# Kernel tuning notes

Measured on AMD Instinct MI355X. Metric: run time of the kernel, lower is better.

The kernel has to match this reference:

```python
import jax, jax.numpy as jnp
import numpy as np

B, S, H, DH = 64, 300, 4, 32   # batch, seq, heads, head_dim
D = H * DH                     # hidden = 128
L = 8                          # num_hidden_layers
SPAN = 8                       # max_relative_positions (att_span)
EPS = 1e-7                     # DebertaConfig layer_norm_eps default


def _ln(x, s, b):
    mu = x.mean(-1, keepdims=True)
    var = ((x - mu) ** 2).mean(-1, keepdims=True)
    return (x - mu) * jax.lax.rsqrt(var + EPS) * s + b


def _gelu(x):
    return jax.nn.gelu(x, approximate=False)  # torch nn.GELU / HF 'gelu' (erf)


def setup_inputs():
    ks = iter(jax.random.split(jax.random.key(0), 48))
    w = lambda shape: jax.random.normal(next(ks), shape, jnp.float32) * 0.02
    return dict(
        inputs=jax.random.uniform(next(ks), (B, S, 4), jnp.float32),
        mask=jnp.ones((B, S), jnp.float32),
        emb_W1=w((3, 64)), emb_b1=w((64,)),
        emb_W2=w((64, D)), emb_b2=w((D,)),
        emb_W3=w((D, D)), emb_b3=w((D,)),
        tok_emb=w((2, D)),
        emb_ln_s=jnp.ones((D,), jnp.float32), emb_ln_b=jnp.zeros((D,), jnp.float32),
        rel_emb=w((2 * SPAN, D)),
        qkv_W=w((L, D, 3 * D)), q_bias=w((L, D)), v_bias=w((L, D)),
        pos_k_W=w((L, D, D)), pos_q_W=w((L, D, D)), pos_q_b=w((L, D)),
        attn_out_W=w((L, D, D)), attn_out_b=w((L, D)),
        ln1_s=jnp.ones((L, D), jnp.float32), ln1_b=jnp.zeros((L, D), jnp.float32),
        ffn_W1=w((L, D, 512)), ffn_b1=w((L, 512)),
        ffn_W2=w((L, 512, D)), ffn_b2=w((L, D)),
        ln2_s=jnp.ones((L, D), jnp.float32), ln2_b=jnp.zeros((L, D), jnp.float32),
        rec_W1=w((D, D)), rec_b1=w((D,)),
        rec_W2=w((D, 64)), rec_b2=w((64,)),
        rec_W3=w((64, 5)), rec_b3=w((5,)),
        conn_W=w((S * 5, 2500)), conn_b=w((2500,)),
    )


def reference(inputs, mask, emb_W1, emb_b1, emb_W2, emb_b2, emb_W3, emb_b3,
              tok_emb, emb_ln_s, emb_ln_b, rel_emb,
              qkv_W, q_bias, v_bias, pos_k_W, pos_q_W, pos_q_b,
              attn_out_W, attn_out_b, ln1_s, ln1_b,
              ffn_W1, ffn_b1, ffn_W2, ffn_b2, ln2_s, ln2_b,
              rec_W1, rec_b1, rec_W2, rec_b2, rec_W3, rec_b3,
              conn_W, conn_b):
    # ---- embedding MLP on first 3 feature columns ----
    e = _gelu(inputs[..., :3] @ emb_W1 + emb_b1)
    e = _gelu(e @ emb_W2 + emb_b2)
    e = _gelu(e @ emb_W3 + emb_b3)
    tok = inputs[..., 3].astype(jnp.int32)            # token_type_ids
    e = _ln(e + tok_emb[tok], emb_ln_s, emb_ln_b)     # position_biased_input=False
    x = e * mask[..., None]                           # DebertaEmbeddings mask mult

    # ---- relative position indices (q_size == k_size == S) ----
    rel = jnp.arange(S)[:, None] - jnp.arange(S)[None, :]
    c2p_idx = jnp.clip(rel + SPAN, 0, 2 * SPAN - 1)   # [S,S]
    p2c_idx = jnp.clip(-rel + SPAN, 0, 2 * SPAN - 1)  # [S,S]
    mask4 = (mask[:, None, :, None] * mask[:, None, None, :]) > 0  # [B,1,S,S]
    neg = jnp.finfo(x.dtype).min
    scale = jnp.sqrt(jnp.asarray(DH * 3, x.dtype))    # scale_factor = 1+len([c2p,p2c])

    for l in range(L):
        qkv = (x @ qkv_W[l]).reshape(B, S, H, 3, DH)  # in_proj (no bias)
        q = qkv[..., 0, :].transpose(0, 2, 1, 3) + q_bias[l].reshape(H, DH)[None, :, None, :]
        k = qkv[..., 1, :].transpose(0, 2, 1, 3)
        v = qkv[..., 2, :].transpose(0, 2, 1, 3) + v_bias[l].reshape(H, DH)[None, :, None, :]
        q = q / scale
        scores = jnp.einsum('bhqd,bhkd->bhqk', q, k)  # content-to-content
        # content-to-position
        pos_k = (rel_emb @ pos_k_W[l]).reshape(2 * SPAN, H, DH).transpose(1, 0, 2)  # [H,16,DH]
        c2p = jnp.einsum('bhqd,hrd->bhqr', q, pos_k)  # [B,H,S,16]
        scores = scores + jnp.take_along_axis(c2p, c2p_idx[None, None], axis=-1)
        # position-to-content
        pos_q = ((rel_emb @ pos_q_W[l]) + pos_q_b[l]).reshape(2 * SPAN, H, DH).transpose(1, 0, 2) / scale
        p2c = jnp.einsum('bhkd,hrd->bhkr', k, pos_q)  # [B,H,S,16]
        scores = scores + jnp.swapaxes(jnp.take_along_axis(p2c, p2c_idx[None, None], axis=-1), -1, -2)
        # XSoftmax
        probs = jnp.where(mask4, jax.nn.softmax(jnp.where(mask4, scores, neg), axis=-1), 0.0)
        ctx = jnp.einsum('bhqk,bhkd->bhqd', probs, v).transpose(0, 2, 1, 3).reshape(B, S, D)
        x = _ln(ctx @ attn_out_W[l] + attn_out_b[l] + x, ln1_s[l], ln1_b[l])
        h = _gelu(x @ ffn_W1[l] + ffn_b1[l])
        x = _ln(h @ ffn_W2[l] + ffn_b2[l] + x, ln2_s[l], ln2_b[l])

    # ---- reconstruction MLP + connection ----
    r = _gelu(x @ rec_W1 + rec_b1)
    r = _gelu(r @ rec_W2 + rec_b2)
    r = _gelu(r @ rec_W3 + rec_b3)                    # [B,S,5]
    out = r.reshape(B, S * 5) @ conn_W + conn_b       # [B,2500]
    return out.reshape(-1, 50, 50)
```

## Files before the change

### kernel.cpp

```cpp
#include <hip/hip_runtime.h>
#include <hip/hip_bf16.h>
#include <math.h>

#define Bq 64
#define Sq 300
#define NH 4
#define DHd 32
#define Dd 128
#define NL 8
#define FF 512
#define NIN 36
#define SP 304
#define SPX 320

typedef __attribute__((ext_vector_type(8))) short bf16x8;
typedef __attribute__((ext_vector_type(4))) float f32x4;

__device__ __forceinline__ float gelu_f(float x) {
    return 0.5f * x * (1.0f + erff(x * 0.70710678118654752f));
}
__device__ __forceinline__ bool bf16_mode(const unsigned* maskw) {
    return maskw[0] == 0x3F803F80u;
}

struct ConvArgs {
    const void* src[NIN];
    float* dst[NIN];
    int n[NIN];
};

__global__ void convert_kernel(ConvArgs a, const unsigned* maskw) {
    bool bfm = bf16_mode(maskw);
    int bi = blockIdx.y;
    int n = a.n[bi];
    float* dst = a.dst[bi];
    int stride = gridDim.x * blockDim.x;
    int i0 = blockIdx.x * blockDim.x + threadIdx.x;
    if (bfm) {
        const __hip_bfloat16* s = (const __hip_bfloat16*)a.src[bi];
        for (int i = i0; i < n; i += stride) dst[i] = __bfloat162float(s[i]);
    } else {
        const float* s = (const float*)a.src[bi];
        for (int i = i0; i < n; i += stride) dst[i] = s[i];
    }
}

__global__ void pack_kernel(const float* __restrict__ W1all, const float* __restrict__ W2all,
                            const float* __restrict__ Wqall, const float* __restrict__ Woall,
                            const float* __restrict__ Wr1, const float* __restrict__ Wr2,
                            const float* __restrict__ We2, const float* __restrict__ We3,
                            __hip_bfloat16* __restrict__ P1, __hip_bfloat16* __restrict__ P2,
                            __hip_bfloat16* __restrict__ Pq, __hip_bfloat16* __restrict__ Po,
                            __hip_bfloat16* __restrict__ Pr1, __hip_bfloat16* __restrict__ Pr2,
                            __hip_bfloat16* __restrict__ Pe2, __hip_bfloat16* __restrict__ Pe3) {
    int l = blockIdx.y;
    int which = blockIdx.z;
    if (which >= 4 && l != 0) return;
    int K = (which == 1) ? 512 : ((which == 6) ? 64 : 128);
    int N = (which == 0) ? 512 : (which == 1 ? 128 : (which == 2 ? 384 : (which == 5 ? 64 : 128)));
    int slots = (K / 32) * (N / 16) * 64;
    int idx = blockIdx.x * 256 + threadIdx.x;
    if (idx >= slots) return;
    int lane = idx & 63;
    int nkt = K / 32;
    int kt = (idx >> 6) % nkt;
    int nt = (idx >> 6) / nkt;
    const float* W; __hip_bfloat16* P;
    switch (which) {
        case 0:  W = W1all + (size_t)l * 128 * 512; P = P1 + (size_t)l * 65536; break;
        case 1:  W = W2all + (size_t)l * 512 * 128; P = P2 + (size_t)l * 65536; break;
        case 2:  W = Wqall + (size_t)l * 128 * 384; P = Pq + (size_t)l * 49152; break;
        case 3:  W = Woall + (size_t)l * 128 * 128; P = Po + (size_t)l * 16384; break;
        case 4:  W = Wr1; P = Pr1; break;
        case 5:  W = Wr2; P = Pr2; break;
        case 6:  W = We2; P = Pe2; break;
        default: W = We3; P = Pe3; break;
    }
    P += (size_t)idx * 8;
    int n = nt * 16 + (lane & 15);
    int k0 = kt * 32 + (lane >> 4) * 8;
    #pragma unroll
    for (int j = 0; j < 8; j++) P[j] = __float2bfloat16(W[(size_t)(k0 + j) * N + n]);
}

__global__ __launch_bounds__(256) void embed_mfma_kernel(
        const float* __restrict__ inp, const float* __restrict__ mask,
        const float* __restrict__ W1, const float* __restrict__ b1,
        const __hip_bfloat16* __restrict__ Pe2, const float* __restrict__ b2,
        const __hip_bfloat16* __restrict__ Pe3, const float* __restrict__ b3,
        const float* __restrict__ tok_emb,
        const float* __restrict__ ln_s, const float* __restrict__ ln_b,
        float* __restrict__ x) {
    int blk = blockIdx.x;
    int t = threadIdx.x;
    int w = t >> 6, lane = t & 63;
    int row0 = blk * 16;
    __shared__ float f[16][4];
    __shared__ __align__(16) __hip_bfloat16 e1a[16 * 72];
    __shared__ __align__(16) __hip_bfloat16 e2a[16 * 136];
    __shared__ float dbuf[16 * 132];
    if (t < 64) f[t >> 2][t & 3] = inp[(size_t)(row0 + (t >> 2)) * 4 + (t & 3)];
    __syncthreads();
    {
        int r1 = t >> 4, n0 = (t & 15) * 4;
        float f0 = f[r1][0], f1 = f[r1][1], f2 = f[r1][2];
        #pragma unroll
        for (int j = 0; j < 4; j++) {
            int n = n0 + j;
            float a = b1[n] + f0 * W1[n] + f1 * W1[64 + n] + f2 * W1[128 + n];
            e1a[r1 * 72 + n] = __float2bfloat16(gelu_f(a));
        }
    }
    __syncthreads();
    int m = lane & 15, quad = lane >> 4;
    bf16x8 a2[2];
    #pragma unroll
    for (int kt = 0; kt < 2; kt++) a2[kt] = *(bf16x8*)&e1a[m * 72 + kt * 32 + quad * 8];
    #pragma unroll
    for (int nt0 = 0; nt0 < 2; nt0++) {
        int nt = w * 2 + nt0;
        f32x4 acc = {0.f, 0.f, 0.f, 0.f};
        const bf16x8* bp = (const bf16x8*)(Pe2 + (size_t)nt * 2 * 512);
        #pragma unroll
        for (int kt = 0; kt < 2; kt++) {
            bf16x8 bfr = bp[kt * 64 + lane];
            acc = __builtin_amdgcn_mfma_f32_16x16x32_bf16(a2[kt], bfr, acc, 0, 0, 0);
        }
        int n = nt * 16 + m;
        float bb = b2[n];
        #pragma unroll
        for (int r = 0; r < 4; r++)
            e2a[(quad * 4 + r) * 136 + n] = __float2bfloat16(gelu_f(acc[r] + bb));
    }
    __syncthreads();
    bf16x8 a3[4];
    #pragma unroll
    for (int kt = 0; kt < 4; kt++) a3[kt] = *(bf16x8*)&e2a[m * 136 + kt * 32 + quad * 8];
    f32x4 acc2[2] = {{0.f,0.f,0.f,0.f}, {0.f,0.f,0.f,0.f}};
    #pragma unroll
    for (int kt = 0; kt < 4; kt++) {
        #pragma unroll
        for (int nt0 = 0; nt0 < 2; nt0++) {
            int nt = w * 2 + nt0;
            bf16x8 bfr = ((const bf16x8*)(Pe3 + (size_t)nt * 4 * 512))[kt * 64 + lane];
            acc2[nt0] = __builtin_amdgcn_mfma_f32_16x16x32_bf16(a3[kt], bfr, acc2[nt0], 0, 0, 0);
        }
    }
    #pragma unroll
    for (int nt0 = 0; nt0 < 2; nt0++) {
        int n = (w * 2 + nt0) * 16 + m;
        float bb = b3[n];
        #pragma unroll
        for (int r = 0; r < 4; r++) {
            int row = quad * 4 + r;
            int tok = (int)f[row][3];
            dbuf[row * 132 + n] = gelu_f(acc2[nt0][r] + bb) + tok_emb[tok * 128 + n];
        }
    }
    __syncthreads();
    #pragma unroll
    for (int rr = 0; rr < 4; rr++) {
        int row = w * 4 + rr;
        int c0 = lane, c1 = lane + 64;
        float y0 = dbuf[row * 132 + c0];
        float y1 = dbuf[row * 132 + c1];
        float sm = y0 + y1;
        #pragma unroll
        for (int o = 32; o > 0; o >>= 1) sm += __shfl_xor(sm, o);
        float mu = sm * (1.0f / 128.0f);
        float d0 = y0 - mu, d1 = y1 - mu;
        float vv = d0 * d0 + d1 * d1;
        #pragma unroll
        for (int o = 32; o > 0; o >>= 1) vv += __shfl_xor(vv, o);
        float rstd = rsqrtf(vv * (1.0f / 128.0f) + 1e-7f);
        float mk = mask[row0 + row];
        x[(size_t)(row0 + row) * 128 + c0] = (d0 * rstd * ln_s[c0] + ln_b[c0]) * mk;
        x[(size_t)(row0 + row) * 128 + c1] = (d1 * rstd * ln_s[c1] + ln_b[c1]) * mk;
    }
}

__global__ __launch_bounds__(256) void qkv_mfma_kernel(const float* __restrict__ x,
                                                       const __hip_bfloat16* __restrict__ Pq,
                                                       const float* __restrict__ qb, const float* __restrict__ vb,
                                                       __hip_bfloat16* __restrict__ qbf,
                                                       __hip_bfloat16* __restrict__ kbf,
                                                       __hip_bfloat16* __restrict__ vT) {
    int blk = blockIdx.x;
    int t = threadIdx.x;
    int w = t >> 6, lane = t & 63;
    int row0 = blk * 16;
    __shared__ __align__(16) __hip_bfloat16 xa[16 * 136];
    for (int i = t; i < 512; i += 256) {
        float4 v4 = ((const float4*)(x + (size_t)row0 * 128))[i];
        int r = i >> 5, c4 = (i & 31) * 4;
        __hip_bfloat16* d = &xa[r * 136 + c4];
        d[0] = __float2bfloat16(v4.x); d[1] = __float2bfloat16(v4.y);
        d[2] = __float2bfloat16(v4.z); d[3] = __float2bfloat16(v4.w);
    }
    __syncthreads();
    int m = lane & 15, quad = lane >> 4;
    bf16x8 a1[4];
    #pragma unroll
    for (int kt = 0; kt < 4; kt++) a1[kt] = *(bf16x8*)&xa[m * 136 + kt * 32 + quad * 8];
    const float inv_scale = 0.10206207261596576f;
    #pragma unroll
    for (int nt0 = 0; nt0 < 6; nt0++) {
        int nt = w * 6 + nt0;
        f32x4 acc = {0.f, 0.f, 0.f, 0.f};
        const bf16x8* bp = (const bf16x8*)(Pq + (size_t)nt * 4 * 512);
        #pragma unroll
        for (int kt = 0; kt < 4; kt++) {
            bf16x8 bfr = bp[kt * 64 + lane];
            acc = __builtin_amdgcn_mfma_f32_16x16x32_bf16(a1[kt], bfr, acc, 0, 0, 0);
        }
        int n = nt * 16 + m;
        int h = n / 96, mm = (n % 96) / 32, d = n % 32;
        float qbv = qb[h * 32 + d], vbv = vb[h * 32 + d];
        #pragma unroll
        for (int r = 0; r < 4; r++) {
            int row = row0 + quad * 4 + r;
            int bb = row / Sq, s = row % Sq;
            int bh = bb * NH + h;
            float a = acc[r];
            if (mm == 0) {
                qbf[((size_t)bh * SP + s) * 32 + d] = __float2bfloat16((a + qbv) * inv_scale);
            } else if (mm == 1) {
                kbf[((size_t)bh * SP + s) * 32 + d] = __float2bfloat16(a);
            } else {
                vT[((size_t)bh * 32 + d) * SP + s] = __float2bfloat16(a + vbv);
            }
        }
    }
}

__global__ void pad_kernel(__hip_bfloat16* qbf, __hip_bfloat16* kbf, __hip_bfloat16* vT) {
    int i = blockIdx.x * 256 + threadIdx.x;
    if (i >= 256 * 4 * 32) return;
    int bh = i >> 7, s = Sq + ((i >> 5) & 3), d = i & 31;
    __hip_bfloat16 z = __float2bfloat16(0.0f);
    qbf[((size_t)bh * SP + s) * 32 + d] = z;
    kbf[((size_t)bh * SP + s) * 32 + d] = z;
    vT[((size_t)bh * 32 + d) * SP + s] = z;
}

__global__ void pos_kernel(const float* __restrict__ rel_emb,
                           const float* __restrict__ pkW_all, const float* __restrict__ pqW_all,
                           const float* __restrict__ pqb_all,
                           __hip_bfloat16* __restrict__ poskb, __hip_bfloat16* __restrict__ posqb) {
    int l = blockIdx.y;
    int bi = blockIdx.x;
    int which = bi >> 4;
    int r = bi & 15;
    int t = threadIdx.x;
    __shared__ float re[128];
    re[t] = rel_emb[r * 128 + t];
    __syncthreads();
    const float* W = (which ? pqW_all : pkW_all) + (size_t)l * 128 * 128;
    float a = 0.0f;
    for (int k = 0; k < 128; k++) a += re[k] * W[k * 128 + t];
    int h = t >> 5, d = t & 31;
    size_t o = ((size_t)(l * NH + h) * 16 + r) * 32 + d;
    if (which) { a = (a + pqb_all[l * 128 + t]) * 0.10206207261596576f; posqb[o] = __float2bfloat16(a); }
    else       { poskb[o] = __float2bfloat16(a); }
}

__global__ __launch_bounds__(256) void attn_mfma_kernel(const __hip_bfloat16* __restrict__ qbf,
                                                        const __hip_bfloat16* __restrict__ kbf,
                                                        const __hip_bfloat16* __restrict__ vT,
                                                        const __hip_bfloat16* __restrict__ poskb,
                                                        const __hip_bfloat16* __restrict__ posqb,
                                                        const float* __restrict__ mask,
                                                        __hip_bfloat16* __restrict__ ctxb) {
    int bh = blockIdx.x;
    int b = bh >> 2, h = bh & 3;
    int t = threadIdx.x;
    int w = t >> 6, lane = t & 63;
    int m = lane & 15, quad = lane >> 4;

    __shared__ float p2cS[SPX * 17];
    __shared__ float c2pS[4][16 * 17];
    __shared__ __align__(16) __hip_bfloat16 pT[4][16 * 40];

    {
        bf16x8 pqf = *(const bf16x8*)&posqb[(h * 16 + m) * 32 + quad * 8];
        #pragma unroll
        for (int it = 0; it < 5; it++) {
            int jb = (w + it * 4) * 16;
            bf16x8 kf2 = *(const bf16x8*)&kbf[((size_t)bh * SP + jb + m) * 32 + quad * 8];
            f32x4 pc = __builtin_amdgcn_mfma_f32_16x16x32_bf16(kf2, pqf, (f32x4){0.f,0.f,0.f,0.f}, 0, 0, 0);
            #pragma unroll
            for (int r = 0; r < 4; r++) {
                int j = jb + quad * 4 + r;
                float mv = (j < Sq) ? mask[b * Sq + j] : 0.0f;
                p2cS[j * 17 + m] = (mv > 0.0f) ? pc[r] : -30000.0f;
            }
        }
    }
    __syncthreads();

    int qt = blockIdx.y * 4 + w;
    if (qt >= 19) return;
    int q0 = qt * 16;

    float* c2pW = c2pS[w];
    __hip_bfloat16* pTW = pT[w];

    bf16x8 aq = *(const bf16x8*)&qbf[((size_t)bh * SP + q0 + m) * 32 + quad * 8];

    {
        bf16x8 pkf = *(const bf16x8*)&poskb[(h * 16 + m) * 32 + quad * 8];
        f32x4 cc = __builtin_amdgcn_mfma_f32_16x16x32_bf16(aq, pkf, (f32x4){0.f,0.f,0.f,0.f}, 0, 0, 0);
        #pragma unroll
        for (int r = 0; r < 4; r++) c2pW[(quad * 4 + r) * 17 + m] = cc[r];
    }

    int qi = q0 + m;
    f32x4 oacc[2] = {{0.f,0.f,0.f,0.f}, {0.f,0.f,0.f,0.f}};
    float lacc = 0.0f;

    for (int jt2 = 0; jt2 < 10; jt2++) {
        int j0 = jt2 * 32;
        #pragma unroll
        for (int half = 0; half < 2; half++) {
            int jh = j0 + half * 16;
            bf16x8 kf = *(const bf16x8*)&kbf[((size_t)bh * SP + jh + m) * 32 + quad * 8];
            f32x4 sc = __builtin_amdgcn_mfma_f32_16x16x32_bf16(kf, aq, (f32x4){0.f,0.f,0.f,0.f}, 0, 0, 0);
            int jb2 = jh + quad * 4;
            int base = qi - jb2 + 8;
            __hip_bfloat16 pb[4];
            #pragma unroll
            for (int r = 0; r < 4; r++) {
                int rr = base - r; rr = rr < 0 ? 0 : (rr > 15 ? 15 : rr);
                float sv = sc[r] + c2pW[m * 17 + rr] + p2cS[(jb2 + r) * 17 + rr];
                float p = __expf(sv);
                lacc += p;
                pb[r] = __float2bfloat16(p);
            }
            *(uint2*)&pTW[m * 40 + half * 16 + quad * 4] = *(uint2*)pb;
        }
        bf16x8 ap = *(bf16x8*)&pTW[m * 40 + quad * 8];
        #pragma unroll
        for (int nt = 0; nt < 2; nt++) {
            bf16x8 vf = *(const bf16x8*)&vT[((size_t)bh * 32 + nt * 16 + m) * SP + j0 + quad * 8];
            oacc[nt] = __builtin_amdgcn_mfma_f32_16x16x32_bf16(ap, vf, oacc[nt], 0, 0, 0);
        }
    }

    lacc += __shfl_xor(lacc, 16);
    lacc += __shfl_xor(lacc, 32);
    #pragma unroll
    for (int r = 0; r < 4; r++) {
        int qrow = quad * 4 + r;
        float lr = __shfl(lacc, qrow);
        int qi2 = q0 + qrow;
        float qm = (qi2 < Sq) ? mask[b * Sq + qi2] : 0.0f;
        float inv = (qm > 0.0f && lr > 0.0f) ? 1.0f / lr : 0.0f;
        if (qi2 < Sq) {
            size_t base2 = ((size_t)(b * Sq + qi2)) * 128 + h * 32;
            ctxb[base2 + m]      = __float2bfloat16(oacc[0][r] * inv);
            ctxb[base2 + 16 + m] = __float2bfloat16(oacc[1][r] * inv);
        }
    }
}

__global__ __launch_bounds__(256) void aoffn_mfma_kernel(
        const __hip_bfloat16* __restrict__ ctxb,
        const __hip_bfloat16* __restrict__ Po, const float* __restrict__ ob,
        const float* __restrict__ ln1s, const float* __restrict__ ln1b,
        const __hip_bfloat16* __restrict__ P1, const float* __restrict__ b1,
        const __hip_bfloat16* __restrict__ P2, const float* __restrict__ b2,
        const float* __restrict__ ln2s, const float* __restrict__ ln2b,
        float* __restrict__ x) {
    int blk = blockIdx.x;
    int t = threadIdx.x;
    int w = t >> 6, lane = t & 63;
    int row0 = blk * 16;

    __shared__ __align__(16) __hip_bfloat16 ca[16 * 136];
    __shared__ float xr[16 * 128];
    __shared__ __align__(16) __hip_bfloat16 ha[16 * 520];
    __shared__ float dbuf[16 * 132];

    {
        uint4 cv = ((const uint4*)(ctxb + (size_t)row0 * 128))[t];
        int r = t >> 4, c8 = (t & 15) * 8;
        *(uint4*)&ca[r * 136 + c8] = cv;
    }
    for (int i = t; i < 512; i += 256) {
        float4 xv4 = ((const float4*)(x + (size_t)row0 * 128))[i];
        int r = i >> 5, c4 = (i & 31) * 4;
        *(float4*)&xr[r * 128 + c4] = xv4;
    }
    __syncthreads();

    int m = lane & 15, quad = lane >> 4;

    {
        bf16x8 a1[4];
        #pragma unroll
        for (int kt = 0; kt < 4; kt++) a1[kt] = *(bf16x8*)&ca[m * 136 + kt * 32 + quad * 8];
        f32x4 acc2[2] = {{0.f,0.f,0.f,0.f}, {0.f,0.f,0.f,0.f}};
        #pragma unroll
        for (int kt = 0; kt < 4; kt++) {
            #pragma unroll
            for (int nt0 = 0; nt0 < 2; nt0++) {
                int nt = w * 2 + nt0;
                bf16x8 bfr = ((const bf16x8*)(Po + (size_t)nt * 4 * 512))[kt * 64 + lane];
                acc2[nt0] = __builtin_amdgcn_mfma_f32_16x16x32_bf16(a1[kt], bfr, acc2[nt0], 0, 0, 0);
            }
        }
        #pragma unroll
        for (int nt0 = 0; nt0 < 2; nt0++) {
            int n = (w * 2 + nt0) * 16 + m;
            #pragma unroll
            for (int r = 0; r < 4; r++) dbuf[(quad * 4 + r) * 132 + n] = acc2[nt0][r];
        }
    }
    __syncthreads();

    #pragma unroll
    for (int rr = 0; rr < 4; rr++) {
        int row = w * 4 + rr;
        int c0 = lane, c1 = lane + 64;
        float y0 = dbuf[row * 132 + c0] + ob[c0] + xr[row * 128 + c0];
        float y1 = dbuf[row * 132 + c1] + ob[c1] + xr[row * 128 + c1];
        float sm = y0 + y1;
        #pragma unroll
        for (int o = 32; o > 0; o >>= 1) sm += __shfl_xor(sm, o);
        float mu = sm * (1.0f / 128.0f);
        float d0 = y0 - mu, d1 = y1 - mu;
        float vv = d0 * d0 + d1 * d1;
        #pragma unroll
        for (int o = 32; o > 0; o >>= 1) vv += __shfl_xor(vv, o);
        float rstd = rsqrtf(vv * (1.0f / 128.0f) + 1e-7f);
        float o0 = d0 * rstd * ln1s[c0] + ln1b[c0];
        float o1 = d1 * rstd * ln1s[c1] + ln1b[c1];
        xr[row * 128 + c0] = o0;
        xr[row * 128 + c1] = o1;
        ca[row * 136 + c0] = __float2bfloat16(o0);
        ca[row * 136 + c1] = __float2bfloat16(o1);
    }
    __syncthreads();

    {
        bf16x8 a1[4];
        #pragma unroll
        for (int kt = 0; kt < 4; kt++) a1[kt] = *(bf16x8*)&ca[m * 136 + kt * 32 + quad * 8];
        #pragma unroll
        for (int nt0 = 0; nt0 < 8; nt0++) {
            int nt = w * 8 + nt0;
            f32x4 acc = {0.f, 0.f, 0.f, 0.f};
            const bf16x8* bp = (const bf16x8*)(P1 + (size_t)nt * 4 * 512);
            #pragma unroll
            for (int kt = 0; kt < 4; kt++) {
                bf16x8 bfr = bp[kt * 64 + lane];
                acc = __builtin_amdgcn_mfma_f32_16x16x32_bf16(a1[kt], bfr, acc, 0, 0, 0);
            }
            int n = nt * 16 + m;
            float bb = b1[n];
            #pragma unroll
            for (int r = 0; r < 4; r++)
                ha[(quad * 4 + r) * 520 + n] = __float2bfloat16(gelu_f(acc[r] + bb));
        }
    }
    __syncthreads();

    {
        f32x4 acc2[2] = {{0.f,0.f,0.f,0.f}, {0.f,0.f,0.f,0.f}};
        #pragma unroll
        for (int kt = 0; kt < 16; kt++) {
            bf16x8 a = *(bf16x8*)&ha[m * 520 + kt * 32 + quad * 8];
            #pragma unroll
            for (int nt0 = 0; nt0 < 2; nt0++) {
                int nt = w * 2 + nt0;
                bf16x8 bfr = ((const bf16x8*)(P2 + (size_t)nt * 16 * 512))[kt * 64 + lane];
                acc2[nt0] = __builtin_amdgcn_mfma_f32_16x16x32_bf16(a, bfr, acc2[nt0], 0, 0, 0);
            }
        }
        #pragma unroll
        for (int nt0 = 0; nt0 < 2; nt0++) {
            int n = (w * 2 + nt0) * 16 + m;
            #pragma unroll
            for (int r = 0; r < 4; r++)
                dbuf[(quad * 4 + r) * 132 + n] = acc2[nt0][r];
        }
    }
    __syncthreads();

    #pragma unroll
    for (int rr = 0; rr < 4; rr++) {
        int row = w * 4 + rr;
        int c0 = lane, c1 = lane + 64;
        float y0 = dbuf[row * 132 + c0] + b2[c0] + xr[row * 128 + c0];
        float y1 = dbuf[row * 132 + c1] + b2[c1] + xr[row * 128 + c1];
        float sm = y0 + y1;
        #pragma unroll
        for (int o = 32; o > 0; o >>= 1) sm += __shfl_xor(sm, o);
        float mu = sm * (1.0f / 128.0f);
        float d0 = y0 - mu, d1 = y1 - mu;
        float vv = d0 * d0 + d1 * d1;
        #pragma unroll
        for (int o = 32; o > 0; o >>= 1) vv += __shfl_xor(vv, o);
        float rstd = rsqrtf(vv * (1.0f / 128.0f) + 1e-7f);
        x[(size_t)(row0 + row) * 128 + c0] = d0 * rstd * ln2s[c0] + ln2b[c0];
        x[(size_t)(row0 + row) * 128 + c1] = d1 * rstd * ln2s[c1] + ln2b[c1];
    }
}

__global__ __launch_bounds__(256) void rec_mfma_kernel(const float* __restrict__ x,
                                                       const __hip_bfloat16* __restrict__ Pr1,
                                                       const float* __restrict__ b1,
                                                       const __hip_bfloat16* __restrict__ Pr2,
                                                       const float* __restrict__ b2,
                                                       const float* __restrict__ W3, const float* __restrict__ b3,
                                                       float* __restrict__ r3) {
    int blk = blockIdx.x;
    int t = threadIdx.x;
    int w = t >> 6, lane = t & 63;
    int row0 = blk * 16;
    __shared__ __align__(16) __hip_bfloat16 xa[16 * 136];
    __shared__ __align__(16) __hip_bfloat16 ha[16 * 136];
    __shared__ float r2s[16 * 68];
    for (int i = t; i < 512; i += 256) {
        float4 v4 = ((const float4*)(x + (size_t)row0 * 128))[i];
        int r = i >> 5, c4 = (i & 31) * 4;
        __hip_bfloat16* d = &xa[r * 136 + c4];
        d[0] = __float2bfloat16(v4.x); d[1] = __float2bfloat16(v4.y);
        d[2] = __float2bfloat16(v4.z); d[3] = __float2bfloat16(v4.w);
    }
    __syncthreads();
    int m = lane & 15, quad = lane >> 4;

    bf16x8 a1[4];
    #pragma unroll
    for (int kt = 0; kt < 4; kt++) a1[kt] = *(bf16x8*)&xa[m * 136 + kt * 32 + quad * 8];
    #pragma unroll
    for (int nt0 = 0; nt0 < 2; nt0++) {
        int nt = w * 2 + nt0;
        f32x4 acc = {0.f, 0.f, 0.f, 0.f};
        const bf16x8* bp = (const bf16x8*)(Pr1 + (size_t)nt * 4 * 512);
        #pragma unroll
        for (int kt = 0; kt < 4; kt++) {
            bf16x8 bfr = bp[kt * 64 + lane];
            acc = __builtin_amdgcn_mfma_f32_16x16x32_bf16(a1[kt], bfr, acc, 0, 0, 0);
        }
        int n = nt * 16 + m;
        float bb = b1[n];
        #pragma unroll
        for (int r = 0; r < 4; r++)
            ha[(quad * 4 + r) * 136 + n] = __float2bfloat16(gelu_f(acc[r] + bb));
    }
    __syncthreads();

    {
        f32x4 acc = {0.f, 0.f, 0.f, 0.f};
        const bf16x8* bp = (const bf16x8*)(Pr2 + (size_t)w * 4 * 512);
        #pragma unroll
        for (int kt = 0; kt < 4; kt++) {
            bf16x8 a = *(bf16x8*)&ha[m * 136 + kt * 32 + quad * 8];
            bf16x8 bfr = bp[kt * 64 + lane];
            acc = __builtin_amdgcn_mfma_f32_16x16x32_bf16(a, bfr, acc, 0, 0, 0);
        }
        int n = w * 16 + m;
        float bb = b2[n];
        #pragma unroll
        for (int r = 0; r < 4; r++)
            r2s[(quad * 4 + r) * 68 + n] = gelu_f(acc[r] + bb);
    }
    __syncthreads();

    if (t < 80) {
        int row = t / 5, c = t % 5;
        float a = b3[c];
        for (int k = 0; k < 64; k++) a += r2s[row * 68 + k] * W3[k * 5 + c];
        r3[(size_t)(row0 + row) * 5 + c] = gelu_f(a);
    }
}

__global__ void conn_kernel(const float* __restrict__ r3, const float* __restrict__ W,
                            const float* __restrict__ b, void* out, const unsigned* maskw) {
    bool bfm = bf16_mode(maskw);
    int cb = blockIdx.x;
    int bg = blockIdx.y;
    int t = threadIdx.x;
    int cl = t & 63;
    int kq = t >> 6;
    int col = cb * 64 + cl;
    __shared__ float rs[4 * 1500];
    __shared__ float pacc[4 * 64 * 4];
    {
        const float4* src = (const float4*)(r3 + (size_t)bg * 4 * 1500);
        for (int i = t; i < 1500; i += 256) ((float4*)rs)[i] = src[i];
    }
    __syncthreads();
    float acc[4] = {0.f, 0.f, 0.f, 0.f};
    if (col < 2500) {
        for (int k = kq * 4; k < 1500; k += 16) {
            float w0 = W[(size_t)(k + 0) * 2500 + col];
            float w1 = W[(size_t)(k + 1) * 2500 + col];
            float w2 = W[(size_t)(k + 2) * 2500 + col];
            float w3 = W[(size_t)(k + 3) * 2500 + col];
            #pragma unroll
            for (int bb = 0; bb < 4; bb++) {
                float4 rv = *(const float4*)&rs[bb * 1500 + k];
                acc[bb] += rv.x * w0 + rv.y * w1 + rv.z * w2 + rv.w * w3;
            }
        }
    }
    #pragma unroll
    for (int bb = 0; bb < 4; bb++) pacc[(kq * 64 + cl) * 4 + bb] = acc[bb];
    __syncthreads();
    if (kq == 0 && col < 2500) {
        float bv = b[col];
        #pragma unroll
        for (int bb = 0; bb < 4; bb++) {
            float a = bv + pacc[(0 * 64 + cl) * 4 + bb] + pacc[(1 * 64 + cl) * 4 + bb]
                         + pacc[(2 * 64 + cl) * 4 + bb] + pacc[(3 * 64 + cl) * 4 + bb];
            int ob = bg * 4 + bb;
            if (bfm) ((__hip_bfloat16*)out)[(size_t)ob * 2500 + col] = __float2bfloat16(a);
            else     ((float*)out)[(size_t)ob * 2500 + col] = a;
        }
    }
}

extern "C" void kernel_launch(void* const* d_in, const int* in_sizes, int n_in,
                              void* d_out, int out_size, void* d_ws, size_t ws_size,
                              hipStream_t stream) {
    float* ws = (float*)d_ws;

    float* cv[NIN];
    size_t off = 0;
    for (int i = 0; i < NIN; i++) { cv[i] = ws + off; off += (size_t)in_sizes[i]; }

    const float* inp      = cv[0];
    const float* mask     = cv[1];
    const float* emb_W1   = cv[2];
    const float* emb_b1   = cv[3];
    const float* emb_W2   = cv[4];
    const float* emb_b2   = cv[5];
    const float* emb_W3   = cv[6];
    const float* emb_b3   = cv[7];
    const float* tok_emb  = cv[8];
    const float* emb_ln_s = cv[9];
    const float* emb_ln_b = cv[10];
    const float* rel_emb  = cv[11];
    const float* qkv_W    = cv[12];
    const float* q_bias   = cv[13];
    const float* v_bias   = cv[14];
    const float* pos_k_W  = cv[15];
    const float* pos_q_W  = cv[16];
    const float* pos_q_b  = cv[17];
    const float* attn_out_W = cv[18];
    const float* attn_out_b = cv[19];
    const float* ln1_s    = cv[20];
    const float* ln1_b    = cv[21];
    const float* ffn_W1   = cv[22];
    const float* ffn_b1   = cv[23];
    const float* ffn_W2   = cv[24];
    const float* ffn_b2   = cv[25];
    const float* ln2_s    = cv[26];
    const float* ln2_b    = cv[27];
    const float* rec_W1   = cv[28];
    const float* rec_b1   = cv[29];
    const float* rec_W2   = cv[30];
    const float* rec_b2   = cv[31];
    const float* rec_W3   = cv[32];
    const float* rec_b3   = cv[33];
    const float* conn_W   = cv[34];
    const float* conn_b   = cv[35];

    const int NTOK = Bq * Sq;
    float* x    = ws + off;
    float* q    = x    + (size_t)NTOK * 128;
    float* k    = q    + (size_t)Bq * NH * Sq * 32;
    float* ctx  = k    + (size_t)Bq * NH * Sq * 32;
    float* c2p  = ctx  + (size_t)NTOK * 128;
    float* p2c  = c2p  + (size_t)Bq * NH * Sq * 16;
    float* posk = p2c  + (size_t)Bq * NH * Sq * 16;
    float* posq = posk + (size_t)NL * 16 * 128;
    float* r3b  = posq + (size_t)NL * 16 * 128;
    float* endf = r3b  + (size_t)NTOK * 5;
    __hip_bfloat16* P1 = (__hip_bfloat16*)endf;
    __hip_bfloat16* P2 = P1 + (size_t)NL * 65536;
    __hip_bfloat16* Pq = P2 + (size_t)NL * 65536;
    __hip_bfloat16* Po = Pq + (size_t)NL * 49152;
    __hip_bfloat16* qbf = Po + (size_t)NL * 16384;
    __hip_bfloat16* kbf = qbf + (size_t)256 * SP * 32;
    __hip_bfloat16* vTb = kbf + (size_t)256 * SP * 32;
    __hip_bfloat16* Pr1 = vTb + (size_t)256 * SP * 32;
    __hip_bfloat16* Pr2 = Pr1 + 16384;
    __hip_bfloat16* Pe2 = Pr2 + 8192;
    __hip_bfloat16* Pe3 = Pe2 + 8192;
    __hip_bfloat16* Pkb = Pe3 + 16384;
    __hip_bfloat16* Pqb = Pkb + (size_t)NL * 2048;
    __hip_bfloat16* ctxb = (__hip_bfloat16*)ctx;

    const unsigned* maskw = (const unsigned*)d_in[1];

    ConvArgs ca;
    for (int i = 0; i < NIN; i++) {
        ca.src[i] = d_in[i];
        ca.dst[i] = cv[i];
        ca.n[i] = in_sizes[i];
    }
    convert_kernel<<<dim3(256, NIN), 256, 0, stream>>>(ca, maskw);
    pack_kernel<<<dim3(32, NL, 8), 256, 0, stream>>>(ffn_W1, ffn_W2, qkv_W, attn_out_W,
                                                     rec_W1, rec_W2, emb_W2, emb_W3,
                                                     P1, P2, Pq, Po, Pr1, Pr2, Pe2, Pe3);

    embed_mfma_kernel<<<NTOK / 16, 256, 0, stream>>>(inp, mask, emb_W1, emb_b1,
                                                     Pe2, emb_b2, Pe3, emb_b3,
                                                     tok_emb, emb_ln_s, emb_ln_b, x);

    pos_kernel<<<dim3(32, NL), 128, 0, stream>>>(rel_emb, pos_k_W, pos_q_W, pos_q_b, Pkb, Pqb);
    pad_kernel<<<128, 256, 0, stream>>>(qbf, kbf, vTb);

    for (int l = 0; l < NL; l++) {
        qkv_mfma_kernel<<<NTOK / 16, 256, 0, stream>>>(x, Pq + (size_t)l * 49152,
                                                       q_bias + l * 128, v_bias + l * 128,
                                                       qbf, kbf, vTb);
        attn_mfma_kernel<<<dim3(256, 5), 256, 0, stream>>>(qbf, kbf, vTb,
                                                           Pkb + (size_t)l * 2048,
                                                           Pqb + (size_t)l * 2048,
                                                           mask, ctxb);
        aoffn_mfma_kernel<<<NTOK / 16, 256, 0, stream>>>(ctxb,
                                                         Po + (size_t)l * 16384, attn_out_b + l * 128,
                                                         ln1_s + l * 128, ln1_b + l * 128,
                                                         P1 + (size_t)l * 65536, ffn_b1 + l * 512,
                                                         P2 + (size_t)l * 65536, ffn_b2 + l * 128,
                                                         ln2_s + l * 128, ln2_b + l * 128, x);
    }

    rec_mfma_kernel<<<NTOK / 16, 256, 0, stream>>>(x, Pr1, rec_b1, Pr2, rec_b2,
                                                   rec_W3, rec_b3, r3b);
    conn_kernel<<<dim3(40, 16), 256, 0, stream>>>(r3b, conn_W, conn_b, d_out, maskw);
}
```

Baseline: 693.2 us.

## Double row tile to 32 in QKV and FFN kernels for weight reuse

The QKV projection and the fused attention-output/FFN kernels now process 32 token rows per block with 512 threads instead of 16 rows with 256. Each wave reuses every loaded weight fragment across two M tiles, which halves the global weight traffic per token. The FFN kernel also stops staging the residual in shared memory, reading it from global memory instead, and overlays the FFN hidden buffer with the output scratch buffer to hold down LDS use. In exchange there are half as many blocks, 600 instead of 1200, more accumulator registers per thread, and an extra barrier.

```diff
diff --git a/kernel.cpp b/kernel.cpp
--- a/kernel.cpp
+++ b/kernel.cpp
@@ -179,7 +179,7 @@
     }
 }
 
-__global__ __launch_bounds__(256) void qkv_mfma_kernel(const float* __restrict__ x,
+__global__ __launch_bounds__(512) void qkv_mfma_kernel(const float* __restrict__ x,
                                                        const __hip_bfloat16* __restrict__ Pq,
                                                        const float* __restrict__ qb, const float* __restrict__ vb,
                                                        __hip_bfloat16* __restrict__ qbf,
@@ -188,9 +188,9 @@
     int blk = blockIdx.x;
     int t = threadIdx.x;
     int w = t >> 6, lane = t & 63;
-    int row0 = blk * 16;
-    __shared__ __align__(16) __hip_bfloat16 xa[16 * 136];
-    for (int i = t; i < 512; i += 256) {
+    int row0 = blk * 32;
+    __shared__ __align__(16) __hip_bfloat16 xa[32 * 136];
+    for (int i = t; i < 1024; i += 512) {
         float4 v4 = ((const float4*)(x + (size_t)row0 * 128))[i];
         int r = i >> 5, c4 = (i & 31) * 4;
         __hip_bfloat16* d = &xa[r * 136 + c4];
@@ -199,35 +199,43 @@
     }
     __syncthreads();
     int m = lane & 15, quad = lane >> 4;
-    bf16x8 a1[4];
-    #pragma unroll
-    for (int kt = 0; kt < 4; kt++) a1[kt] = *(bf16x8*)&xa[m * 136 + kt * 32 + quad * 8];
+    bf16x8 a1[2][4];
+    #pragma unroll
+    for (int mt = 0; mt < 2; mt++)
+        #pragma unroll
+        for (int kt = 0; kt < 4; kt++)
+            a1[mt][kt] = *(bf16x8*)&xa[(mt * 16 + m) * 136 + kt * 32 + quad * 8];
     const float inv_scale = 0.10206207261596576f;
     #pragma unroll
-    for (int nt0 = 0; nt0 < 6; nt0++) {
-        int nt = w * 6 + nt0;
-        f32x4 acc = {0.f, 0.f, 0.f, 0.f};
+    for (int nt0 = 0; nt0 < 3; nt0++) {
+        int nt = w * 3 + nt0;
+        f32x4 acc[2] = {{0.f,0.f,0.f,0.f}, {0.f,0.f,0.f,0.f}};
         const bf16x8* bp = (const bf16x8*)(Pq + (size_t)nt * 4 * 512);
         #pragma unroll
         for (int kt = 0; kt < 4; kt++) {
             bf16x8 bfr = bp[kt * 64 + lane];
-            acc = __builtin_amdgcn_mfma_f32_16x16x32_bf16(a1[kt], bfr, acc, 0, 0, 0);
+            #pragma unroll
+            for (int mt = 0; mt < 2; mt++)
+                acc[mt] = __builtin_amdgcn_mfma_f32_16x16x32_bf16(a1[mt][kt], bfr, acc[mt], 0, 0, 0);
         }
         int n = nt * 16 + m;
         int h = n / 96, mm = (n % 96) / 32, d = n % 32;
         float qbv = qb[h * 32 + d], vbv = vb[h * 32 + d];
         #pragma unroll
-        for (int r = 0; r < 4; r++) {
-            int row = row0 + quad * 4 + r;
-            int bb = row / Sq, s = row % Sq;
-            int bh = bb * NH + h;
-            float a = acc[r];
-            if (mm == 0) {
-                qbf[((size_t)bh * SP + s) * 32 + d] = __float2bfloat16((a + qbv) * inv_scale);
-            } else if (mm == 1) {
-                kbf[((size_t)bh * SP + s) * 32 + d] = __float2bfloat16(a);
-            } else {
-                vT[((size_t)bh * 32 + d) * SP + s] = __float2bfloat16(a + vbv);
+        for (int mt = 0; mt < 2; mt++) {
+            #pragma unroll
+            for (int r = 0; r < 4; r++) {
+                int row = row0 + mt * 16 + quad * 4 + r;
+                int bb = row / Sq, s = row % Sq;
+                int bh = bb * NH + h;
+                float a = acc[mt][r];
+                if (mm == 0) {
+                    qbf[((size_t)bh * SP + s) * 32 + d] = __float2bfloat16((a + qbv) * inv_scale);
+                } else if (mm == 1) {
+                    kbf[((size_t)bh * SP + s) * 32 + d] = __float2bfloat16(a);
+                } else {
+                    vT[((size_t)bh * 32 + d) * SP + s] = __float2bfloat16(a + vbv);
+                }
             }
         }
     }
@@ -363,7 +371,7 @@
     }
 }
 
-__global__ __launch_bounds__(256) void aoffn_mfma_kernel(
+__global__ __launch_bounds__(512) void aoffn_mfma_kernel(
         const __hip_bfloat16* __restrict__ ctxb,
         const __hip_bfloat16* __restrict__ Po, const float* __restrict__ ob,
         const float* __restrict__ ln1s, const float* __restrict__ ln1b,
@@ -374,47 +382,41 @@
     int blk = blockIdx.x;
     int t = threadIdx.x;
     int w = t >> 6, lane = t & 63;
-    int row0 = blk * 16;
-
-    __shared__ __align__(16) __hip_bfloat16 ca[16 * 136];
-    __shared__ float xr[16 * 128];
-    __shared__ __align__(16) __hip_bfloat16 ha[16 * 520];
-    __shared__ float dbuf[16 * 132];
+    int row0 = blk * 32;
+
+    __shared__ __align__(16) __hip_bfloat16 ca[32 * 136];
+    __shared__ float xr[32 * 128];
+    __shared__ __align__(16) char hbuf[32 * 520 * 2];
+    __hip_bfloat16* ha = (__hip_bfloat16*)hbuf;
+    float* dbuf = (float*)hbuf;
 
     {
         uint4 cv = ((const uint4*)(ctxb + (size_t)row0 * 128))[t];
         int r = t >> 4, c8 = (t & 15) * 8;
         *(uint4*)&ca[r * 136 + c8] = cv;
     }
-    for (int i = t; i < 512; i += 256) {
-        float4 xv4 = ((const float4*)(x + (size_t)row0 * 128))[i];
-        int r = i >> 5, c4 = (i & 31) * 4;
-        *(float4*)&xr[r * 128 + c4] = xv4;
-    }
     __syncthreads();
 
     int m = lane & 15, quad = lane >> 4;
 
     {
-        bf16x8 a1[4];
-        #pragma unroll
-        for (int kt = 0; kt < 4; kt++) a1[kt] = *(bf16x8*)&ca[m * 136 + kt * 32 + quad * 8];
-        f32x4 acc2[2] = {{0.f,0.f,0.f,0.f}, {0.f,0.f,0.f,0.f}};
+        f32x4 acc[2] = {{0.f,0.f,0.f,0.f}, {0.f,0.f,0.f,0.f}};
+        const bf16x8* bp = (const bf16x8*)(Po + (size_t)w * 4 * 512);
         #pragma unroll
         for (int kt = 0; kt < 4; kt++) {
-            #pragma unroll
-            for (int nt0 = 0; nt0 < 2; nt0++) {
-                int nt = w * 2 + nt0;
-                bf16x8 bfr = ((const bf16x8*)(Po + (size_t)nt * 4 * 512))[kt * 64 + lane];
-                acc2[nt0] = __builtin_amdgcn_mfma_f32_16x16x32_bf16(a1[kt], bfr, acc2[nt0], 0, 0, 0);
+            bf16x8 bfr = bp[kt * 64 + lane];
+            #pragma unroll
+            for (int mt = 0; mt < 2; mt++) {
+                bf16x8 a = *(bf16x8*)&ca[(mt * 16 + m) * 136 + kt * 32 + quad * 8];
+                acc[mt] = __builtin_amdgcn_mfma_f32_16x16x32_bf16(a, bfr, acc[mt], 0, 0, 0);
             }
         }
-        #pragma unroll
-        for (int nt0 = 0; nt0 < 2; nt0++) {
-            int n = (w * 2 + nt0) * 16 + m;
-            #pragma unroll
-            for (int r = 0; r < 4; r++) dbuf[(quad * 4 + r) * 132 + n] = acc2[nt0][r];
-        }
+        int n = w * 16 + m;
+        #pragma unroll
+        for (int mt = 0; mt < 2; mt++)
+            #pragma unroll
+            for (int r = 0; r < 4; r++)
+                dbuf[(mt * 16 + quad * 4 + r) * 132 + n] = acc[mt][r];
     }
     __syncthreads();
 
@@ -422,8 +424,9 @@
     for (int rr = 0; rr < 4; rr++) {
         int row = w * 4 + rr;
         int c0 = lane, c1 = lane + 64;
-        float y0 = dbuf[row * 132 + c0] + ob[c0] + xr[row * 128 + c0];
-        float y1 = dbuf[row * 132 + c1] + ob[c1] + xr[row * 128 + c1];
+        size_t g = (size_t)(row0 + row) * 128;
+        float y0 = dbuf[row * 132 + c0] + ob[c0] + x[g + c0];
+        float y1 = dbuf[row * 132 + c1] + ob[c1] + x[g + c1];
         float sm = y0 + y1;
         #pragma unroll
         for (int o = 32; o > 0; o >>= 1) sm += __shfl_xor(sm, o);
@@ -443,47 +446,56 @@
     __syncthreads();
 
     {
-        bf16x8 a1[4];
-        #pragma unroll
-        for (int kt = 0; kt < 4; kt++) a1[kt] = *(bf16x8*)&ca[m * 136 + kt * 32 + quad * 8];
-        #pragma unroll
-        for (int nt0 = 0; nt0 < 8; nt0++) {
-            int nt = w * 8 + nt0;
-            f32x4 acc = {0.f, 0.f, 0.f, 0.f};
+        bf16x8 a1[2][4];
+        #pragma unroll
+        for (int mt = 0; mt < 2; mt++)
+            #pragma unroll
+            for (int kt = 0; kt < 4; kt++)
+                a1[mt][kt] = *(bf16x8*)&ca[(mt * 16 + m) * 136 + kt * 32 + quad * 8];
+        #pragma unroll
+        for (int nt0 = 0; nt0 < 4; nt0++) {
+            int nt = w * 4 + nt0;
+            f32x4 acc[2] = {{0.f,0.f,0.f,0.f}, {0.f,0.f,0.f,0.f}};
             const bf16x8* bp = (const bf16x8*)(P1 + (size_t)nt * 4 * 512);
             #pragma unroll
             for (int kt = 0; kt < 4; kt++) {
                 bf16x8 bfr = bp[kt * 64 + lane];
-                acc = __builtin_amdgcn_mfma_f32_16x16x32_bf16(a1[kt], bfr, acc, 0, 0, 0);
+                #pragma unroll
+                for (int mt = 0; mt < 2; mt++)
+                    acc[mt] = __builtin_amdgcn_mfma_f32_16x16x32_bf16(a1[mt][kt], bfr, acc[mt], 0, 0, 0);
             }
             int n = nt * 16 + m;
             float bb = b1[n];
             #pragma unroll
+            for (int mt = 0; mt < 2; mt++)
+                #pragma unroll
+                for (int r = 0; r < 4; r++)
+                    ha[(mt * 16 + quad * 4 + r) * 520 + n] = __float2bfloat16(gelu_f(acc[mt][r] + bb));
+        }
+    }
+    __syncthreads();
+
+    f32x4 acc2[2] = {{0.f,0.f,0.f,0.f}, {0.f,0.f,0.f,0.f}};
+    {
+        const bf16x8* bp = (const bf16x8*)(P2 + (size_t)w * 16 * 512);
+        #pragma unroll
+        for (int kt = 0; kt < 16; kt++) {
+            bf16x8 bfr = bp[kt * 64 + lane];
+            #pragma unroll
+            for (int mt = 0; mt < 2; mt++) {
+                bf16x8 a = *(bf16x8*)&ha[(mt * 16 + m) * 520 + kt * 32 + quad * 8];
+                acc2[mt] = __builtin_amdgcn_mfma_f32_16x16x32_bf16(a, bfr, acc2[mt], 0, 0, 0);
+            }
+        }
+    }
+    __syncthreads();
+    {
+        int n = w * 16 + m;
+        #pragma unroll
+        for (int mt = 0; mt < 2; mt++)
+            #pragma unroll
             for (int r = 0; r < 4; r++)
-                ha[(quad * 4 + r) * 520 + n] = __float2bfloat16(gelu_f(acc[r] + bb));
-        }
-    }
-    __syncthreads();
-
-    {
-        f32x4 acc2[2] = {{0.f,0.f,0.f,0.f}, {0.f,0.f,0.f,0.f}};
-        #pragma unroll
-        for (int kt = 0; kt < 16; kt++) {
-            bf16x8 a = *(bf16x8*)&ha[m * 520 + kt * 32 + quad * 8];
-            #pragma unroll
-            for (int nt0 = 0; nt0 < 2; nt0++) {
-                int nt = w * 2 + nt0;
-                bf16x8 bfr = ((const bf16x8*)(P2 + (size_t)nt * 16 * 512))[kt * 64 + lane];
-                acc2[nt0] = __builtin_amdgcn_mfma_f32_16x16x32_bf16(a, bfr, acc2[nt0], 0, 0, 0);
-            }
-        }
-        #pragma unroll
-        for (int nt0 = 0; nt0 < 2; nt0++) {
-            int n = (w * 2 + nt0) * 16 + m;
-            #pragma unroll
-            for (int r = 0; r < 4; r++)
-                dbuf[(quad * 4 + r) * 132 + n] = acc2[nt0][r];
-        }
+                dbuf[(mt * 16 + quad * 4 + r) * 132 + n] = acc2[mt][r];
     }
     __syncthreads();
 
@@ -716,14 +728,14 @@
     pad_kernel<<<128, 256, 0, stream>>>(qbf, kbf, vTb);
 
     for (int l = 0; l < NL; l++) {
-        qkv_mfma_kernel<<<NTOK / 16, 256, 0, stream>>>(x, Pq + (size_t)l * 49152,
+        qkv_mfma_kernel<<<NTOK / 32, 512, 0, stream>>>(x, Pq + (size_t)l * 49152,
                                                        q_bias + l * 128, v_bias + l * 128,
                                                        qbf, kbf, vTb);
         attn_mfma_kernel<<<dim3(256, 5), 256, 0, stream>>>(qbf, kbf, vTb,
                                                            Pkb + (size_t)l * 2048,
                                                            Pqb + (size_t)l * 2048,
                                                            mask, ctxb);
-        aoffn_mfma_kernel<<<NTOK / 16, 256, 0, stream>>>(ctxb,
+        aoffn_mfma_kernel<<<NTOK / 32, 512, 0, stream>>>(ctxb,
                                                          Po + (size_t)l * 16384, attn_out_b + l * 128,
                                                          ln1_s + l * 128, ln1_b + l * 128,
                                                          P1 + (size_t)l * 65536, ffn_b1 + l * 512,
```

After: 697.1 us. Within noise of the previous version (+0.6%).
